# Performance work log

Hardware: AMD Instinct MI355X
Metric: run time of the kernel (lower is better)

## Reference

```python
import jax, jax.numpy as jnp
import numpy as np

B, LE, LS, DE, DS = 16, 1024, 1024, 1024, 1024


def setup_inputs() -> dict:
    key = jax.random.key(0)
    k1, k2, k3 = jax.random.split(key, 3)
    edit_encodings = jax.random.normal(k1, (B, LE, DE), dtype=jnp.float32)
    src_encodings = jax.random.normal(k2, (B, LS, DS), dtype=jnp.float32)
    # torch nn.Linear(DE, DS, bias=False) weight has shape (DS, DE)
    W = jax.random.normal(k3, (DS, DE), dtype=jnp.float32) * (1.0 / np.sqrt(DE))
    # padding masks: 1 for padding. Per-example valid lengths in [L/2, L].
    edit_lens = np.linspace(LE // 2, LE, B).astype(np.int32)
    src_lens = np.linspace(LS, LS // 2, B).astype(np.int32)
    edit_sent_masks = (np.arange(LE)[None, :] >= edit_lens[:, None]).astype(np.int32)
    src_sent_masks = (np.arange(LS)[None, :] >= src_lens[:, None]).astype(np.int32)
    return {
        "edit_encodings": edit_encodings,
        "src_encodings": src_encodings,
        "edit_sent_masks": jnp.asarray(edit_sent_masks),
        "src_sent_masks": jnp.asarray(src_sent_masks),
        "W": W,
    }


def reference(edit_encodings, src_encodings, edit_sent_masks, src_sent_masks, W):
    # sim: (B, LE, LS) = (edit @ W^T) @ src^T
    proj = jnp.einsum('bed,sd->bes', edit_encodings, W)          # (B, LE, DS)
    sim = jnp.einsum('bes,bls->bel', proj, src_encodings)        # (B, LE, LS)
    neg_inf = jnp.float32(-jnp.inf)
    edit_sim = jnp.where(src_sent_masks[:, None, :].astype(bool), neg_inf, sim)
    src_sim = jnp.where(edit_sent_masks[:, :, None].astype(bool), neg_inf, sim)
    edit_weights = jax.nn.softmax(edit_sim, axis=-1)             # over src positions
    src_weights = jax.nn.softmax(src_sim, axis=1)                # over edit positions
    edit_ctx = jnp.einsum('bel,bls->bes', edit_weights, src_encodings)  # (B, LE, DS)
    src_ctx = jnp.einsum('bel,bed->bld', src_weights, edit_encodings)   # (B, LS, DE)
    return (edit_ctx, src_ctx)
```

## Files before the change

### kernel.cpp

```cpp
#include <hip/hip_runtime.h>
#include <math.h>

#define BATCH 16

typedef __attribute__((ext_vector_type(8))) short s16x8;
typedef __attribute__((ext_vector_type(8))) unsigned short u16x8;
typedef __attribute__((ext_vector_type(4))) float f32x4;

__device__ inline unsigned short f2bf_rn(float f) {
  unsigned u = __float_as_uint(f);
  u += 0x7FFF + ((u >> 16) & 1);
  return (unsigned short)(u >> 16);
}
__device__ inline float bf2f(unsigned short h) {
  return __uint_as_float(((unsigned)h) << 16);
}

#define LDK 40

__global__ __launch_bounds__(256) void cvt_split(
    const float* __restrict__ X, unsigned short* __restrict__ H,
    unsigned short* __restrict__ L) {
  const size_t i = (((size_t)blockIdx.x << 8) + threadIdx.x) << 2;
  f32x4 v = *(const f32x4*)(X + i);
  ushort4 h, l;
  h.x = f2bf_rn(v[0]); l.x = f2bf_rn(v[0] - bf2f(h.x));
  h.y = f2bf_rn(v[1]); l.y = f2bf_rn(v[1] - bf2f(h.y));
  h.z = f2bf_rn(v[2]); l.z = f2bf_rn(v[2] - bf2f(h.z));
  h.w = f2bf_rn(v[3]); l.w = f2bf_rn(v[3] - bf2f(h.w));
  *(ushort4*)(H + i) = h;
  *(ushort4*)(L + i) = l;
}

template <int SPLIT_OUT>
__global__ __launch_bounds__(256) void gemm_split3b(
    const unsigned short* __restrict__ AH, const unsigned short* __restrict__ AL,
    const unsigned short* __restrict__ BH, const unsigned short* __restrict__ BL,
    void* __restrict__ Cout, void* __restrict__ CoutL,
    long long sA, long long sB, long long sC) {
  __shared__ unsigned short Ahs[128 * LDK], Als[128 * LDK];
  __shared__ unsigned short Bhs[128 * LDK], Bls[128 * LDK];
  const int z = blockIdx.z;
  const size_t oA = (size_t)z * sA, oB = (size_t)z * sB;
  const int tid = threadIdx.x;
  const int bm = blockIdx.x << 7, bn = blockIdx.y << 7;
  const int wave = tid >> 6, lane = tid & 63;
  const int wm = (wave & 1) << 6, wn = (wave >> 1) << 6;
  const int fr = lane & 15, fk = (lane >> 4) << 3;

  f32x4 acc[4][4];
#pragma unroll
  for (int i = 0; i < 4; i++)
#pragma unroll
    for (int j = 0; j < 4; j++) acc[i][j] = (f32x4)(0.f);

  const int sr = tid >> 1, sk = (tid & 1) << 4;
  const unsigned short* pAH = AH + oA + (size_t)(bm + sr) * 1024 + sk;
  const unsigned short* pAL = AL + oA + (size_t)(bm + sr) * 1024 + sk;
  const unsigned short* pBH = BH + oB + (size_t)(bn + sr) * 1024 + sk;
  const unsigned short* pBL = BL + oB + (size_t)(bn + sr) * 1024 + sk;
  unsigned short* wAh = &Ahs[sr * LDK + sk];
  unsigned short* wAl = &Als[sr * LDK + sk];
  unsigned short* wBh = &Bhs[sr * LDK + sk];
  unsigned short* wBl = &Bls[sr * LDK + sk];

#pragma unroll 1
  for (int k0 = 0; k0 < 1024; k0 += 32) {
    u16x8 ah0 = *(const u16x8*)(pAH + k0), ah1 = *(const u16x8*)(pAH + k0 + 8);
    u16x8 al0 = *(const u16x8*)(pAL + k0), al1 = *(const u16x8*)(pAL + k0 + 8);
    u16x8 bh0 = *(const u16x8*)(pBH + k0), bh1 = *(const u16x8*)(pBH + k0 + 8);
    u16x8 bl0 = *(const u16x8*)(pBL + k0), bl1 = *(const u16x8*)(pBL + k0 + 8);
    __syncthreads();
    *(u16x8*)(wAh) = ah0; *(u16x8*)(wAh + 8) = ah1;
    *(u16x8*)(wAl) = al0; *(u16x8*)(wAl + 8) = al1;
    *(u16x8*)(wBh) = bh0; *(u16x8*)(wBh + 8) = bh1;
    *(u16x8*)(wBl) = bl0; *(u16x8*)(wBl + 8) = bl1;
    __syncthreads();

    s16x8 ah[4], al[4];
#pragma unroll
    for (int i = 0; i < 4; i++) {
      const int ro = (wm + (i << 4) + fr) * LDK + fk;
      ah[i] = *(const s16x8*)&Ahs[ro];
      al[i] = *(const s16x8*)&Als[ro];
    }
#pragma unroll
    for (int j = 0; j < 4; j++) {
      const int ro = (wn + (j << 4) + fr) * LDK + fk;
      s16x8 bh = *(const s16x8*)&Bhs[ro];
      s16x8 bl = *(const s16x8*)&Bls[ro];
#pragma unroll
      for (int i = 0; i < 4; i++) {
        acc[i][j] = __builtin_amdgcn_mfma_f32_16x16x32_bf16(al[i], bh, acc[i][j], 0, 0, 0);
        acc[i][j] = __builtin_amdgcn_mfma_f32_16x16x32_bf16(ah[i], bl, acc[i][j], 0, 0, 0);
        acc[i][j] = __builtin_amdgcn_mfma_f32_16x16x32_bf16(ah[i], bh, acc[i][j], 0, 0, 0);
      }
    }
  }
  const int cr = (lane >> 4) << 2;
  if (SPLIT_OUT) {
    unsigned short* CH = (unsigned short*)Cout + (size_t)z * sC;
    unsigned short* CL = (unsigned short*)CoutL + (size_t)z * sC;
#pragma unroll
    for (int i = 0; i < 4; i++)
#pragma unroll
      for (int r = 0; r < 4; r++) {
        size_t base = (size_t)(bm + wm + (i << 4) + cr + r) * 1024 + bn + wn + fr;
#pragma unroll
        for (int j = 0; j < 4; j++) {
          float f = acc[i][j][r];
          unsigned short h = f2bf_rn(f);
          CH[base + (j << 4)] = h;
          CL[base + (j << 4)] = f2bf_rn(f - bf2f(h));
        }
      }
  } else {
    float* C = (float*)Cout + (size_t)z * sC;
#pragma unroll
    for (int i = 0; i < 4; i++)
#pragma unroll
      for (int r = 0; r < 4; r++) {
        float* cp = C + (size_t)(bm + wm + (i << 4) + cr + r) * 1024 + bn + wn + fr;
#pragma unroll
        for (int j = 0; j < 4; j++) cp[j << 4] = acc[i][j][r];
      }
  }
}

__global__ __launch_bounds__(256) void gemm_bf16(
    const unsigned short* __restrict__ A, const unsigned short* __restrict__ B,
    float* __restrict__ C, long long sA, long long sB, long long sC) {
  __shared__ unsigned short Ah[128 * LDK];
  __shared__ unsigned short Bh[128 * LDK];
  const int z = blockIdx.z;
  A += (size_t)z * sA; B += (size_t)z * sB; C += (size_t)z * sC;
  const int tid = threadIdx.x;
  const int bm = blockIdx.x << 7, bn = blockIdx.y << 7;
  const int wave = tid >> 6, lane = tid & 63;
  const int wm = (wave & 1) << 6, wn = (wave >> 1) << 6;
  const int fr = lane & 15, fk = (lane >> 4) << 3;

  f32x4 acc[4][4];
#pragma unroll
  for (int i = 0; i < 4; i++)
#pragma unroll
    for (int j = 0; j < 4; j++) acc[i][j] = (f32x4)(0.f);

  const int sr = tid >> 1, sk = (tid & 1) << 4;
  const unsigned short* pA = A + (size_t)(bm + sr) * 1024 + sk;
  const unsigned short* pB = B + (size_t)(bn + sr) * 1024 + sk;
  unsigned short* sAh = &Ah[sr * LDK + sk];
  unsigned short* sBh = &Bh[sr * LDK + sk];

#pragma unroll 1
  for (int k0 = 0; k0 < 1024; k0 += 32) {
    u16x8 a0 = *(const u16x8*)(pA + k0), a1 = *(const u16x8*)(pA + k0 + 8);
    u16x8 b0 = *(const u16x8*)(pB + k0), b1 = *(const u16x8*)(pB + k0 + 8);
    __syncthreads();
    *(u16x8*)(sAh) = a0; *(u16x8*)(sAh + 8) = a1;
    *(u16x8*)(sBh) = b0; *(u16x8*)(sBh + 8) = b1;
    __syncthreads();

    s16x8 ah[4];
#pragma unroll
    for (int i = 0; i < 4; i++)
      ah[i] = *(const s16x8*)&Ah[(wm + (i << 4) + fr) * LDK + fk];
#pragma unroll
    for (int j = 0; j < 4; j++) {
      s16x8 bh = *(const s16x8*)&Bh[(wn + (j << 4) + fr) * LDK + fk];
#pragma unroll
      for (int i = 0; i < 4; i++)
        acc[i][j] = __builtin_amdgcn_mfma_f32_16x16x32_bf16(ah[i], bh, acc[i][j], 0, 0, 0);
    }
  }
  const int cr = (lane >> 4) << 2;
#pragma unroll
  for (int i = 0; i < 4; i++)
#pragma unroll
    for (int r = 0; r < 4; r++) {
      float* cp = C + (size_t)(bm + wm + (i << 4) + cr + r) * 1024 + bn + wn + fr;
#pragma unroll
      for (int j = 0; j < 4; j++) cp[j << 4] = acc[i][j][r];
    }
}

__device__ inline float waveMax(float v) {
#pragma unroll
  for (int o = 32; o > 0; o >>= 1) v = fmaxf(v, __shfl_down(v, o, 64));
  return v;
}
__device__ inline float waveSum(float v) {
#pragma unroll
  for (int o = 32; o > 0; o >>= 1) v += __shfl_down(v, o, 64);
  return v;
}

__global__ __launch_bounds__(256) void row_softmax_kernel(
    const float* __restrict__ sim, const int* __restrict__ smask,
    unsigned short* __restrict__ out) {
  const int row = blockIdx.x;
  const int b = row >> 10;
  const float* x = sim + ((size_t)row << 10);
  const int* mk = smask + (b << 10);
  const int t = threadIdx.x;

  float4 v = ((const float4*)x)[t];
  int4 m = ((const int4*)mk)[t];
  float vv[4] = {v.x, v.y, v.z, v.w};
  const int mmv[4] = {m.x, m.y, m.z, m.w};

  float mx = -3.0e38f;
#pragma unroll
  for (int i = 0; i < 4; i++)
    if (!mmv[i]) mx = fmaxf(mx, vv[i]);

  __shared__ float red[4];
  float wmx = waveMax(mx);
  const int wave = t >> 6;
  if ((t & 63) == 0) red[wave] = wmx;
  __syncthreads();
  mx = fmaxf(fmaxf(red[0], red[1]), fmaxf(red[2], red[3]));
  __syncthreads();

  float s = 0.f;
#pragma unroll
  for (int i = 0; i < 4; i++) {
    float e = mmv[i] ? 0.f : __expf(vv[i] - mx);
    vv[i] = e;
    s += e;
  }
  float ws = waveSum(s);
  if ((t & 63) == 0) red[wave] = ws;
  __syncthreads();
  s = red[0] + red[1] + red[2] + red[3];
  float inv = 1.0f / s;

  ushort4 o;
  o.x = f2bf_rn(vv[0] * inv);
  o.y = f2bf_rn(vv[1] * inv);
  o.z = f2bf_rn(vv[2] * inv);
  o.w = f2bf_rn(vv[3] * inv);
  *(ushort4*)&out[((size_t)row << 10) + (t << 2)] = o;
}

__global__ __launch_bounds__(256) void col_partial(
    const float* __restrict__ sim, const int* __restrict__ emask,
    float* __restrict__ pmax, float* __restrict__ psum) {
  const int b = blockIdx.z;
  const int ec = blockIdx.y;
  const int l = (blockIdx.x << 8) + threadIdx.x;
  const float* p = sim + ((size_t)b << 20) + (((size_t)ec << 6) << 10) + l;
  const int* mk = emask + (b << 10) + (ec << 6);
  float mx0 = -1.0e30f, s0 = 0.f, mx1 = -1.0e30f, s1 = 0.f;
#pragma unroll 4
  for (int i = 0; i < 64; i += 2) {
    float v0 = mk[i] ? -3.0e38f : p[(size_t)i << 10];
    float v1 = mk[i + 1] ? -3.0e38f : p[(size_t)(i + 1) << 10];
    float n0 = fmaxf(mx0, v0);
    s0 = s0 * __expf(mx0 - n0) + __expf(v0 - n0);
    mx0 = n0;
    float n1 = fmaxf(mx1, v1);
    s1 = s1 * __expf(mx1 - n1) + __expf(v1 - n1);
    mx1 = n1;
  }
  float M = fmaxf(mx0, mx1);
  float S = s0 * __expf(mx0 - M) + s1 * __expf(mx1 - M);
  const int o = (((b << 4) + ec) << 10) + l;
  pmax[o] = M;
  psum[o] = S;
}

__global__ __launch_bounds__(256) void col_weights_T(
    const float* __restrict__ sim, const int* __restrict__ emask,
    const float* __restrict__ pmax, const float* __restrict__ psum,
    unsigned short* __restrict__ wT) {
  const int b = blockIdx.z;
  const int l0 = blockIdx.x << 6;
  const int e0 = blockIdx.y << 6;
  const int t = threadIdx.x;
  __shared__ float Ml[64], Il[64];
  __shared__ int msk[64];
  __shared__ float gm[4][64], gs[4][64];
  __shared__ unsigned short tile[64][72];

  {
    const int ll = t & 63, g = t >> 6;
    float m = -1.0e30f, s = 0.f;
#pragma unroll
    for (int q = 0; q < 4; q++) {
      int ec = g + (q << 2);
      const int o = (((b << 4) + ec) << 10) + l0 + ll;
      float pm = pmax[o], ps = psum[o];
      float nm = fmaxf(m, pm);
      s = s * __expf(m - nm) + ps * __expf(pm - nm);
      m = nm;
    }
    gm[g][ll] = m;
    gs[g][ll] = s;
    __syncthreads();
    if (t < 64) {
      float M = fmaxf(fmaxf(gm[0][t], gm[1][t]), fmaxf(gm[2][t], gm[3][t]));
      float S = 0.f;
#pragma unroll
      for (int q = 0; q < 4; q++) S += gs[q][t] * __expf(gm[q][t] - M);
      Ml[t] = M;
      Il[t] = 1.0f / S;
      msk[t] = emask[(b << 10) + e0 + t];
    }
    __syncthreads();
  }

  const int lane = t & 63, wv = t >> 6;
#pragma unroll
  for (int i = 0; i < 16; i++) {
    const int el = (wv << 4) + i;
    float v = sim[((size_t)b << 20) + ((size_t)(e0 + el) << 10) + l0 + lane];
    float w = msk[el] ? 0.f : __expf(v - Ml[lane]) * Il[lane];
    tile[lane][el] = f2bf_rn(w);
  }
  __syncthreads();
  const int r = t >> 2, seg = (t & 3) << 4;
  u16x8 v0 = *(const u16x8*)&tile[r][seg];
  u16x8 v1 = *(const u16x8*)&tile[r][seg + 8];
  size_t o = ((size_t)((b << 10) + l0 + r) << 10) + e0 + seg;
  *(u16x8*)&wT[o] = v0;
  *(u16x8*)&wT[o + 8] = v1;
}

__global__ __launch_bounds__(256) void transpose16(
    const unsigned short* __restrict__ X, unsigned short* __restrict__ XT) {
  __shared__ unsigned short ts[64][72];
  const int b = blockIdx.z;
  const int d0 = blockIdx.x << 6, l0 = blockIdx.y << 6;
  const int t = threadIdx.x;
  const unsigned short* Xb = X + ((size_t)b << 20);
  unsigned short* Tb = XT + ((size_t)b << 20);
  const int row = t >> 2, seg = (t & 3) << 4;
  u16x8 v0 = *(const u16x8*)&Xb[((size_t)(l0 + row) << 10) + d0 + seg];
  u16x8 v1 = *(const u16x8*)&Xb[((size_t)(l0 + row) << 10) + d0 + seg + 8];
#pragma unroll
  for (int i = 0; i < 8; i++) ts[seg + i][row] = v0[i];
#pragma unroll
  for (int i = 0; i < 8; i++) ts[seg + 8 + i][row] = v1[i];
  __syncthreads();
  u16x8 o0 = *(const u16x8*)&ts[row][seg];
  u16x8 o1 = *(const u16x8*)&ts[row][seg + 8];
  size_t o = ((size_t)(d0 + row) << 10) + l0 + seg;
  *(u16x8*)&Tb[o] = o0;
  *(u16x8*)&Tb[o + 8] = o1;
}

extern "C" void kernel_launch(void* const* d_in, const int* in_sizes, int n_in,
                              void* d_out, int out_size, void* d_ws,
                              size_t ws_size, hipStream_t stream) {
  const float* edit = (const float*)d_in[0];
  const float* src = (const float*)d_in[1];
  const int* emask = (const int*)d_in[2];
  const int* smask = (const int*)d_in[3];
  const float* W = (const float*)d_in[4];

  char* ws = (char*)d_ws;
  char* dob = (char*)d_out;

  unsigned short* eH = (unsigned short*)ws;
  unsigned short* sH = (unsigned short*)(ws + ((size_t)32 << 20));
  unsigned short* pH = (unsigned short*)(ws + ((size_t)64 << 20));
  unsigned short* pL = (unsigned short*)(ws + ((size_t)96 << 20));
  unsigned short* wE = pH;
  unsigned short* wST = pL;
  unsigned short* editT = sH;

  unsigned short* eL = (unsigned short*)dob;
  unsigned short* sL = (unsigned short*)(dob + ((size_t)64 << 20));
  unsigned short* WH = (unsigned short*)(dob + ((size_t)96 << 20));
  unsigned short* WL = (unsigned short*)(dob + ((size_t)98 << 20));
  float* sim = (float*)dob;
  float* pmax = (float*)(dob + ((size_t)64 << 20));
  float* psum = (float*)(dob + ((size_t)65 << 20));
  unsigned short* srcT = (unsigned short*)(dob + ((size_t)64 << 20));
  float* out_edit = (float*)dob;
  float* out_src = (float*)(dob + ((size_t)64 << 20));

  const long long S1 = 1LL << 20;
  dim3 blk(256);

  cvt_split<<<dim3(16384), blk, 0, stream>>>(edit, eH, eL);
  cvt_split<<<dim3(16384), blk, 0, stream>>>(src, sH, sL);
  cvt_split<<<dim3(1024), blk, 0, stream>>>(W, WH, WL);

  gemm_split3b<1><<<dim3(128, 8, 1), blk, 0, stream>>>(
      eH, eL, WH, WL, (void*)pH, (void*)pL, 0, 0, 0);

  gemm_split3b<0><<<dim3(8, 8, BATCH), blk, 0, stream>>>(
      pH, pL, sH, sL, (void*)sim, nullptr, S1, S1, S1);

  row_softmax_kernel<<<dim3(BATCH << 10), blk, 0, stream>>>(sim, smask, wE);
  col_partial<<<dim3(4, 16, BATCH), blk, 0, stream>>>(sim, emask, pmax, psum);
  col_weights_T<<<dim3(16, 16, BATCH), blk, 0, stream>>>(sim, emask, pmax, psum, wST);

  transpose16<<<dim3(16, 16, BATCH), blk, 0, stream>>>(sH, srcT);
  transpose16<<<dim3(16, 16, BATCH), blk, 0, stream>>>(eH, editT);

  gemm_bf16<<<dim3(8, 8, BATCH), blk, 0, stream>>>(wE, srcT, out_edit, S1, S1, S1);
  gemm_bf16<<<dim3(8, 8, BATCH), blk, 0, stream>>>(wST, editT, out_src, S1, S1, S1);
}
```

Measured before the change: 666.6 us.

## Use direct global-to-LDS loads with XOR swizzle and XCD-aware block remap in GEMMs

The GEMM kernels now stage tiles with global_load_lds (direct global-to-LDS DMA) instead of loading into registers and then writing to shared memory. The padded LDK=40 layout is replaced by an unpadded 32-wide layout with an XOR swizzle to avoid LDS bank conflicts. The grid is flattened to 1D and block indices are remapped so that consecutive tiles land on the same XCD, improving L2 reuse. The cost is a fixed swizzle mapping and a dependence on the global_load_lds builtin and its 16-byte width support.

```diff
diff --git a/kernel.cpp b/kernel.cpp
--- a/kernel.cpp
+++ b/kernel.cpp
@@ -16,7 +16,11 @@
   return __uint_as_float(((unsigned)h) << 16);
 }
 
-#define LDK 40
+__device__ __forceinline__ void gload16(const unsigned short* g, unsigned short* l) {
+  __builtin_amdgcn_global_load_lds(
+      (__attribute__((address_space(1))) void*)g,
+      (__attribute__((address_space(3))) void*)l, 16, 0, 0);
+}
 
 __global__ __launch_bounds__(256) void cvt_split(
     const float* __restrict__ X, unsigned short* __restrict__ H,
@@ -38,15 +42,20 @@
     const unsigned short* __restrict__ BH, const unsigned short* __restrict__ BL,
     void* __restrict__ Cout, void* __restrict__ CoutL,
     long long sA, long long sB, long long sC) {
-  __shared__ unsigned short Ahs[128 * LDK], Als[128 * LDK];
-  __shared__ unsigned short Bhs[128 * LDK], Bls[128 * LDK];
-  const int z = blockIdx.z;
+  __shared__ unsigned short Ahs[128 * 32], Als[128 * 32];
+  __shared__ unsigned short Bhs[128 * 32], Bls[128 * 32];
+  const int tid = threadIdx.x;
+  const int wg = ((blockIdx.x & 7) << 7) | (blockIdx.x >> 3);
+  int bm, bn, z;
+  if (SPLIT_OUT) {
+    z = 0; bm = (wg >> 3) << 7; bn = (wg & 7) << 7;
+  } else {
+    z = wg >> 6; bm = ((wg >> 3) & 7) << 7; bn = (wg & 7) << 7;
+  }
   const size_t oA = (size_t)z * sA, oB = (size_t)z * sB;
-  const int tid = threadIdx.x;
-  const int bm = blockIdx.x << 7, bn = blockIdx.y << 7;
   const int wave = tid >> 6, lane = tid & 63;
   const int wm = (wave & 1) << 6, wn = (wave >> 1) << 6;
-  const int fr = lane & 15, fk = (lane >> 4) << 3;
+  const int fr = lane & 15, fks = lane >> 4;
 
   f32x4 acc[4][4];
 #pragma unroll
@@ -54,41 +63,49 @@
 #pragma unroll
     for (int j = 0; j < 4; j++) acc[i][j] = (f32x4)(0.f);
 
-  const int sr = tid >> 1, sk = (tid & 1) << 4;
-  const unsigned short* pAH = AH + oA + (size_t)(bm + sr) * 1024 + sk;
-  const unsigned short* pAL = AL + oA + (size_t)(bm + sr) * 1024 + sk;
-  const unsigned short* pBH = BH + oB + (size_t)(bn + sr) * 1024 + sk;
-  const unsigned short* pBL = BL + oB + (size_t)(bn + sr) * 1024 + sk;
-  unsigned short* wAh = &Ahs[sr * LDK + sk];
-  unsigned short* wAl = &Als[sr * LDK + sk];
-  unsigned short* wBh = &Bhs[sr * LDK + sk];
-  unsigned short* wBl = &Bls[sr * LDK + sk];
+  const int srow = (wave << 5) + (lane >> 2);
+  const int gso = ((lane & 3) ^ ((srow >> 1) & 3)) << 3;
+  const unsigned short* gAH = AH + oA + (size_t)(bm + srow) * 1024 + gso;
+  const unsigned short* gAL = AL + oA + (size_t)(bm + srow) * 1024 + gso;
+  const unsigned short* gBH = BH + oB + (size_t)(bn + srow) * 1024 + gso;
+  const unsigned short* gBL = BL + oB + (size_t)(bn + srow) * 1024 + gso;
+  unsigned short* lAh = Ahs + (wave << 10);
+  unsigned short* lAl = Als + (wave << 10);
+  unsigned short* lBh = Bhs + (wave << 10);
+  unsigned short* lBl = Bls + (wave << 10);
+
+  int roA[4], roB[4];
+#pragma unroll
+  for (int i = 0; i < 4; i++) {
+    int rr = wm + (i << 4) + fr;
+    roA[i] = rr * 32 + ((fks ^ ((rr >> 1) & 3)) << 3);
+    rr = wn + (i << 4) + fr;
+    roB[i] = rr * 32 + ((fks ^ ((rr >> 1) & 3)) << 3);
+  }
 
 #pragma unroll 1
   for (int k0 = 0; k0 < 1024; k0 += 32) {
-    u16x8 ah0 = *(const u16x8*)(pAH + k0), ah1 = *(const u16x8*)(pAH + k0 + 8);
-    u16x8 al0 = *(const u16x8*)(pAL + k0), al1 = *(const u16x8*)(pAL + k0 + 8);
-    u16x8 bh0 = *(const u16x8*)(pBH + k0), bh1 = *(const u16x8*)(pBH + k0 + 8);
-    u16x8 bl0 = *(const u16x8*)(pBL + k0), bl1 = *(const u16x8*)(pBL + k0 + 8);
-    __syncthreads();
-    *(u16x8*)(wAh) = ah0; *(u16x8*)(wAh + 8) = ah1;
-    *(u16x8*)(wAl) = al0; *(u16x8*)(wAl + 8) = al1;
-    *(u16x8*)(wBh) = bh0; *(u16x8*)(wBh + 8) = bh1;
-    *(u16x8*)(wBl) = bl0; *(u16x8*)(wBl + 8) = bl1;
+    __syncthreads();
+    gload16(gAH + k0, lAh);
+    gload16(gAH + k0 + 16384, lAh + 512);
+    gload16(gAL + k0, lAl);
+    gload16(gAL + k0 + 16384, lAl + 512);
+    gload16(gBH + k0, lBh);
+    gload16(gBH + k0 + 16384, lBh + 512);
+    gload16(gBL + k0, lBl);
+    gload16(gBL + k0 + 16384, lBl + 512);
     __syncthreads();
 
     s16x8 ah[4], al[4];
 #pragma unroll
     for (int i = 0; i < 4; i++) {
-      const int ro = (wm + (i << 4) + fr) * LDK + fk;
-      ah[i] = *(const s16x8*)&Ahs[ro];
-      al[i] = *(const s16x8*)&Als[ro];
+      ah[i] = *(const s16x8*)&Ahs[roA[i]];
+      al[i] = *(const s16x8*)&Als[roA[i]];
     }
 #pragma unroll
     for (int j = 0; j < 4; j++) {
-      const int ro = (wn + (j << 4) + fr) * LDK + fk;
-      s16x8 bh = *(const s16x8*)&Bhs[ro];
-      s16x8 bl = *(const s16x8*)&Bls[ro];
+      s16x8 bh = *(const s16x8*)&Bhs[roB[j]];
+      s16x8 bl = *(const s16x8*)&Bls[roB[j]];
 #pragma unroll
       for (int i = 0; i < 4; i++) {
         acc[i][j] = __builtin_amdgcn_mfma_f32_16x16x32_bf16(al[i], bh, acc[i][j], 0, 0, 0);
@@ -130,15 +147,16 @@
 __global__ __launch_bounds__(256) void gemm_bf16(
     const unsigned short* __restrict__ A, const unsigned short* __restrict__ B,
     float* __restrict__ C, long long sA, long long sB, long long sC) {
-  __shared__ unsigned short Ah[128 * LDK];
-  __shared__ unsigned short Bh[128 * LDK];
-  const int z = blockIdx.z;
+  __shared__ unsigned short Ahs[128 * 32];
+  __shared__ unsigned short Bhs[128 * 32];
+  const int tid = threadIdx.x;
+  const int wg = ((blockIdx.x & 7) << 7) | (blockIdx.x >> 3);
+  const int z = wg >> 6;
+  const int bm = ((wg >> 3) & 7) << 7, bn = (wg & 7) << 7;
   A += (size_t)z * sA; B += (size_t)z * sB; C += (size_t)z * sC;
-  const int tid = threadIdx.x;
-  const int bm = blockIdx.x << 7, bn = blockIdx.y << 7;
   const int wave = tid >> 6, lane = tid & 63;
   const int wm = (wave & 1) << 6, wn = (wave >> 1) << 6;
-  const int fr = lane & 15, fk = (lane >> 4) << 3;
+  const int fr = lane & 15, fks = lane >> 4;
 
   f32x4 acc[4][4];
 #pragma unroll
@@ -146,28 +164,37 @@
 #pragma unroll
     for (int j = 0; j < 4; j++) acc[i][j] = (f32x4)(0.f);
 
-  const int sr = tid >> 1, sk = (tid & 1) << 4;
-  const unsigned short* pA = A + (size_t)(bm + sr) * 1024 + sk;
-  const unsigned short* pB = B + (size_t)(bn + sr) * 1024 + sk;
-  unsigned short* sAh = &Ah[sr * LDK + sk];
-  unsigned short* sBh = &Bh[sr * LDK + sk];
+  const int srow = (wave << 5) + (lane >> 2);
+  const int gso = ((lane & 3) ^ ((srow >> 1) & 3)) << 3;
+  const unsigned short* gA = A + (size_t)(bm + srow) * 1024 + gso;
+  const unsigned short* gB = B + (size_t)(bn + srow) * 1024 + gso;
+  unsigned short* lA = Ahs + (wave << 10);
+  unsigned short* lB = Bhs + (wave << 10);
+
+  int roA[4], roB[4];
+#pragma unroll
+  for (int i = 0; i < 4; i++) {
+    int rr = wm + (i << 4) + fr;
+    roA[i] = rr * 32 + ((fks ^ ((rr >> 1) & 3)) << 3);
+    rr = wn + (i << 4) + fr;
+    roB[i] = rr * 32 + ((fks ^ ((rr >> 1) & 3)) << 3);
+  }
 
 #pragma unroll 1
   for (int k0 = 0; k0 < 1024; k0 += 32) {
-    u16x8 a0 = *(const u16x8*)(pA + k0), a1 = *(const u16x8*)(pA + k0 + 8);
-    u16x8 b0 = *(const u16x8*)(pB + k0), b1 = *(const u16x8*)(pB + k0 + 8);
-    __syncthreads();
-    *(u16x8*)(sAh) = a0; *(u16x8*)(sAh + 8) = a1;
-    *(u16x8*)(sBh) = b0; *(u16x8*)(sBh + 8) = b1;
+    __syncthreads();
+    gload16(gA + k0, lA);
+    gload16(gA + k0 + 16384, lA + 512);
+    gload16(gB + k0, lB);
+    gload16(gB + k0 + 16384, lB + 512);
     __syncthreads();
 
     s16x8 ah[4];
 #pragma unroll
-    for (int i = 0; i < 4; i++)
-      ah[i] = *(const s16x8*)&Ah[(wm + (i << 4) + fr) * LDK + fk];
+    for (int i = 0; i < 4; i++) ah[i] = *(const s16x8*)&Ahs[roA[i]];
 #pragma unroll
     for (int j = 0; j < 4; j++) {
-      s16x8 bh = *(const s16x8*)&Bh[(wn + (j << 4) + fr) * LDK + fk];
+      s16x8 bh = *(const s16x8*)&Bhs[roB[j]];
 #pragma unroll
       for (int i = 0; i < 4; i++)
         acc[i][j] = __builtin_amdgcn_mfma_f32_16x16x32_bf16(ah[i], bh, acc[i][j], 0, 0, 0);
@@ -388,10 +415,10 @@
   cvt_split<<<dim3(16384), blk, 0, stream>>>(src, sH, sL);
   cvt_split<<<dim3(1024), blk, 0, stream>>>(W, WH, WL);
 
-  gemm_split3b<1><<<dim3(128, 8, 1), blk, 0, stream>>>(
+  gemm_split3b<1><<<dim3(1024), blk, 0, stream>>>(
       eH, eL, WH, WL, (void*)pH, (void*)pL, 0, 0, 0);
 
-  gemm_split3b<0><<<dim3(8, 8, BATCH), blk, 0, stream>>>(
+  gemm_split3b<0><<<dim3(1024), blk, 0, stream>>>(
       pH, pL, sH, sL, (void*)sim, nullptr, S1, S1, S1);
 
   row_softmax_kernel<<<dim3(BATCH << 10), blk, 0, stream>>>(sim, smask, wE);
@@ -401,6 +428,6 @@
   transpose16<<<dim3(16, 16, BATCH), blk, 0, stream>>>(sH, srcT);
   transpose16<<<dim3(16, 16, BATCH), blk, 0, stream>>>(eH, editT);
 
-  gemm_bf16<<<dim3(8, 8, BATCH), blk, 0, stream>>>(wE, srcT, out_edit, S1, S1, S1);
-  gemm_bf16<<<dim3(8, 8, BATCH), blk, 0, stream>>>(wST, editT, out_src, S1, S1, S1);
-}
+  gemm_bf16<<<dim3(1024), blk, 0, stream>>>(wE, srcT, out_edit, S1, S1, S1);
+  gemm_bf16<<<dim3(1024), blk, 0, stream>>>(wST, editT, out_src, S1, S1, S1);
+}
```

After: 621.9 us. 6.7% less time.

## Replace GEMMs with 256x256 double-buffered direct-to-LDS MFMA kernel and merge launches

Applied to the files above, without the earlier changes.

Replaces both GEMM kernels with one templated 512-thread kernel that computes 256x256 tiles. It double-buffers LDS through global_load_lds, uses an XOR-swizzled LDS layout, interleaves prefetch with MFMA phases using s_barrier and setprio, and remaps block indices for locality. It also merges the two conversion launches and the two transpose launches into single kernels. The aim is more data reuse per tile, hiding global load latency and cutting launch overhead. The cost is higher register and LDS use, and only 256 workgroups per GEMM, which may leave some CUs underused.

```diff
diff --git a/kernel.cpp b/kernel.cpp
--- a/kernel.cpp
+++ b/kernel.cpp
@@ -16,7 +16,11 @@
   return __uint_as_float(((unsigned)h) << 16);
 }
 
-#define LDK 40
+__device__ __forceinline__ void gload16(const unsigned short* g, unsigned short* l) {
+  __builtin_amdgcn_global_load_lds(
+      (__attribute__((address_space(1))) void*)g,
+      (__attribute__((address_space(3))) void*)l, 16, 0, 0);
+}
 
 __global__ __launch_bounds__(256) void cvt_split(
     const float* __restrict__ X, unsigned short* __restrict__ H,
@@ -32,156 +36,190 @@
   *(ushort4*)(L + i) = l;
 }
 
-template <int SPLIT_OUT>
-__global__ __launch_bounds__(256) void gemm_split3b(
+__global__ __launch_bounds__(256) void cvt_split2(
+    const float* __restrict__ X0, unsigned short* __restrict__ H0,
+    unsigned short* __restrict__ L0, const float* __restrict__ X1,
+    unsigned short* __restrict__ H1, unsigned short* __restrict__ L1) {
+  const int bid = blockIdx.x;
+  const float* X;
+  unsigned short *H, *L;
+  size_t base;
+  if (bid < 16384) { X = X0; H = H0; L = L0; base = (size_t)bid << 8; }
+  else { X = X1; H = H1; L = L1; base = (size_t)(bid - 16384) << 8; }
+  const size_t i = (base + threadIdx.x) << 2;
+  f32x4 v = *(const f32x4*)(X + i);
+  ushort4 h, l;
+  h.x = f2bf_rn(v[0]); l.x = f2bf_rn(v[0] - bf2f(h.x));
+  h.y = f2bf_rn(v[1]); l.y = f2bf_rn(v[1] - bf2f(h.y));
+  h.z = f2bf_rn(v[2]); l.z = f2bf_rn(v[2] - bf2f(h.z));
+  h.w = f2bf_rn(v[3]); l.w = f2bf_rn(v[3] - bf2f(h.w));
+  *(ushort4*)(H + i) = h;
+  *(ushort4*)(L + i) = l;
+}
+
+template <int HILO, int SPLIT_OUT>
+__global__ __launch_bounds__(512, 2) void gemm8p(
     const unsigned short* __restrict__ AH, const unsigned short* __restrict__ AL,
     const unsigned short* __restrict__ BH, const unsigned short* __restrict__ BL,
     void* __restrict__ Cout, void* __restrict__ CoutL,
-    long long sA, long long sB, long long sC) {
-  __shared__ unsigned short Ahs[128 * LDK], Als[128 * LDK];
-  __shared__ unsigned short Bhs[128 * LDK], Bls[128 * LDK];
-  const int z = blockIdx.z;
-  const size_t oA = (size_t)z * sA, oB = (size_t)z * sB;
+    long long sA, long long sB, long long sC, int batched) {
+  constexpr int NARR = HILO ? 4 : 2;
+  __shared__ __align__(16) unsigned short lds[2][NARR][8192];
   const int tid = threadIdx.x;
-  const int bm = blockIdx.x << 7, bn = blockIdx.y << 7;
+  const int wg = ((blockIdx.x & 7) << 5) | (blockIdx.x >> 3);
+  int z, bm, bn;
+  if (batched) {
+    z = wg >> 4; bm = ((wg >> 2) & 3) << 8; bn = (wg & 3) << 8;
+  } else {
+    z = 0; bm = (wg >> 2) << 8; bn = (wg & 3) << 8;
+  }
   const int wave = tid >> 6, lane = tid & 63;
-  const int wm = (wave & 1) << 6, wn = (wave >> 1) << 6;
-  const int fr = lane & 15, fk = (lane >> 4) << 3;
-
-  f32x4 acc[4][4];
-#pragma unroll
-  for (int i = 0; i < 4; i++)
-#pragma unroll
-    for (int j = 0; j < 4; j++) acc[i][j] = (f32x4)(0.f);
-
-  const int sr = tid >> 1, sk = (tid & 1) << 4;
-  const unsigned short* pAH = AH + oA + (size_t)(bm + sr) * 1024 + sk;
-  const unsigned short* pAL = AL + oA + (size_t)(bm + sr) * 1024 + sk;
-  const unsigned short* pBH = BH + oB + (size_t)(bn + sr) * 1024 + sk;
-  const unsigned short* pBL = BL + oB + (size_t)(bn + sr) * 1024 + sk;
-  unsigned short* wAh = &Ahs[sr * LDK + sk];
-  unsigned short* wAl = &Als[sr * LDK + sk];
-  unsigned short* wBh = &Bhs[sr * LDK + sk];
-  unsigned short* wBl = &Bls[sr * LDK + sk];
+  const int wm = wave >> 2, wn = wave & 3;
+  const int fr = lane & 15, fks = lane >> 4;
+
+  const int svrow = tid >> 2;
+  const int scol = ((tid & 3) ^ ((tid >> 3) & 3)) << 3;
+  const unsigned short* gA0 = AH + (size_t)z * sA + (size_t)(bm + svrow) * 1024 + scol;
+  const unsigned short* gB0 = BH + (size_t)z * sB + (size_t)(bn + svrow) * 1024 + scol;
+  const unsigned short* gA1 = HILO ? (AL + (size_t)z * sA + (size_t)(bm + svrow) * 1024 + scol) : gA0;
+  const unsigned short* gB1 = HILO ? (BL + (size_t)z * sB + (size_t)(bn + svrow) * 1024 + scol) : gB0;
+  const int lwb = wave << 9;
+
+  int aoff[8], boff[4];
+#pragma unroll
+  for (int m = 0; m < 8; m++) {
+    const int r = (wm << 7) + (m << 4) + fr;
+    aoff[m] = (r << 5) + ((fks ^ ((r >> 1) & 3)) << 3);
+  }
+#pragma unroll
+  for (int n = 0; n < 4; n++) {
+    const int r = (wn << 6) + (n << 4) + fr;
+    boff[n] = (r << 5) + ((fks ^ ((r >> 1) & 3)) << 3);
+  }
+
+  f32x4 acc[8][4];
+#pragma unroll
+  for (int m = 0; m < 8; m++)
+#pragma unroll
+    for (int n = 0; n < 4; n++) acc[m][n] = (f32x4)(0.f);
+
+#define ISS(NXT, ARR, G, Q, KO) \
+  gload16((G) + ((size_t)(Q) << 17) + (KO), &lds[NXT][ARR][((Q) << 12) + lwb])
+
+  ISS(0, 0, gA0, 0, 0); ISS(0, 0, gA0, 1, 0);
+  ISS(0, 1, gB0, 0, 0); ISS(0, 1, gB0, 1, 0);
+  if (HILO) {
+    ISS(0, 2, gA1, 0, 0); ISS(0, 2, gA1, 1, 0);
+    ISS(0, 3, gB1, 0, 0); ISS(0, 3, gB1, 1, 0);
+  }
+  __syncthreads();
 
 #pragma unroll 1
-  for (int k0 = 0; k0 < 1024; k0 += 32) {
-    u16x8 ah0 = *(const u16x8*)(pAH + k0), ah1 = *(const u16x8*)(pAH + k0 + 8);
-    u16x8 al0 = *(const u16x8*)(pAL + k0), al1 = *(const u16x8*)(pAL + k0 + 8);
-    u16x8 bh0 = *(const u16x8*)(pBH + k0), bh1 = *(const u16x8*)(pBH + k0 + 8);
-    u16x8 bl0 = *(const u16x8*)(pBL + k0), bl1 = *(const u16x8*)(pBL + k0 + 8);
+  for (int kt = 0; kt < 32; ++kt) {
+    const int cur = kt & 1, nxt = cur ^ 1;
+    const int kn = (kt + 1) << 5;
+    const bool pf = kt < 31;
+    const unsigned short* LAH = lds[cur][0];
+    const unsigned short* LBH = lds[cur][1];
+    const unsigned short* LAL = lds[cur][HILO ? 2 : 0];
+    const unsigned short* LBL = lds[cur][HILO ? 3 : 1];
+    s16x8 ah[4], al[4], bh[2], bl[2];
+
+#define LDA8(QM)                                                         \
+  do {                                                                   \
+    _Pragma("unroll") for (int m_ = 0; m_ < 4; m_++) {                   \
+      const int o_ = aoff[((QM) << 2) + m_];                             \
+      ah[m_] = *(const s16x8*)&LAH[o_];                                  \
+      if (HILO) al[m_] = *(const s16x8*)&LAL[o_];                        \
+    }                                                                    \
+  } while (0)
+#define LDB4(QN)                                                         \
+  do {                                                                   \
+    _Pragma("unroll") for (int n_ = 0; n_ < 2; n_++) {                   \
+      const int o_ = boff[((QN) << 1) + n_];                             \
+      bh[n_] = *(const s16x8*)&LBH[o_];                                  \
+      if (HILO) bl[n_] = *(const s16x8*)&LBL[o_];                        \
+    }                                                                    \
+  } while (0)
+#define MM8(QM, QN)                                                              \
+  do {                                                                           \
+    _Pragma("unroll") for (int m_ = 0; m_ < 4; m_++)                             \
+        _Pragma("unroll") for (int n_ = 0; n_ < 2; n_++) {                       \
+      const int M_ = ((QM) << 2) + m_, N_ = ((QN) << 1) + n_;                    \
+      if (HILO) {                                                                \
+        acc[M_][N_] = __builtin_amdgcn_mfma_f32_16x16x32_bf16(al[m_], bh[n_],    \
+                                                              acc[M_][N_], 0, 0, 0); \
+        acc[M_][N_] = __builtin_amdgcn_mfma_f32_16x16x32_bf16(ah[m_], bl[n_],    \
+                                                              acc[M_][N_], 0, 0, 0); \
+      }                                                                          \
+      acc[M_][N_] = __builtin_amdgcn_mfma_f32_16x16x32_bf16(ah[m_], bh[n_],      \
+                                                            acc[M_][N_], 0, 0, 0);   \
+    }                                                                            \
+  } while (0)
+
+    LDA8(0); LDB4(0);
+    if (pf) {
+      ISS(nxt, 0, gA0, 0, kn); ISS(nxt, 0, gA0, 1, kn);
+      if (HILO) { ISS(nxt, 2, gA1, 0, kn); ISS(nxt, 2, gA1, 1, kn); }
+    }
+    __builtin_amdgcn_s_barrier();
+    __builtin_amdgcn_s_setprio(1); MM8(0, 0); __builtin_amdgcn_s_setprio(0);
+    __builtin_amdgcn_s_barrier();
+
+    LDB4(1);
+    if (pf) {
+      ISS(nxt, 1, gB0, 0, kn); ISS(nxt, 1, gB0, 1, kn);
+      if (HILO) { ISS(nxt, 3, gB1, 0, kn); ISS(nxt, 3, gB1, 1, kn); }
+    }
+    __builtin_amdgcn_s_barrier();
+    __builtin_amdgcn_s_setprio(1); MM8(0, 1); __builtin_amdgcn_s_setprio(0);
+    __builtin_amdgcn_s_barrier();
+
+    LDA8(1); LDB4(0);
+    __builtin_amdgcn_s_barrier();
+    __builtin_amdgcn_s_setprio(1); MM8(1, 0); __builtin_amdgcn_s_setprio(0);
+    __builtin_amdgcn_s_barrier();
+
+    LDB4(1);
+    __builtin_amdgcn_s_barrier();
+    __builtin_amdgcn_s_setprio(1); MM8(1, 1); __builtin_amdgcn_s_setprio(0);
     __syncthreads();
-    *(u16x8*)(wAh) = ah0; *(u16x8*)(wAh + 8) = ah1;
-    *(u16x8*)(wAl) = al0; *(u16x8*)(wAl + 8) = al1;
-    *(u16x8*)(wBh) = bh0; *(u16x8*)(wBh + 8) = bh1;
-    *(u16x8*)(wBl) = bl0; *(u16x8*)(wBl + 8) = bl1;
-    __syncthreads();
-
-    s16x8 ah[4], al[4];
-#pragma unroll
-    for (int i = 0; i < 4; i++) {
-      const int ro = (wm + (i << 4) + fr) * LDK + fk;
-      ah[i] = *(const s16x8*)&Ahs[ro];
-      al[i] = *(const s16x8*)&Als[ro];
-    }
-#pragma unroll
-    for (int j = 0; j < 4; j++) {
-      const int ro = (wn + (j << 4) + fr) * LDK + fk;
-      s16x8 bh = *(const s16x8*)&Bhs[ro];
-      s16x8 bl = *(const s16x8*)&Bls[ro];
-#pragma unroll
-      for (int i = 0; i < 4; i++) {
-        acc[i][j] = __builtin_amdgcn_mfma_f32_16x16x32_bf16(al[i], bh, acc[i][j], 0, 0, 0);
-        acc[i][j] = __builtin_amdgcn_mfma_f32_16x16x32_bf16(ah[i], bl, acc[i][j], 0, 0, 0);
-        acc[i][j] = __builtin_amdgcn_mfma_f32_16x16x32_bf16(ah[i], bh, acc[i][j], 0, 0, 0);
-      }
-    }
-  }
+#undef LDA8
+#undef LDB4
+#undef MM8
+  }
+#undef ISS
+
   const int cr = (lane >> 4) << 2;
+  const int crow0 = bm + (wm << 7);
+  const int ccol0 = bn + (wn << 6);
   if (SPLIT_OUT) {
     unsigned short* CH = (unsigned short*)Cout + (size_t)z * sC;
     unsigned short* CL = (unsigned short*)CoutL + (size_t)z * sC;
 #pragma unroll
-    for (int i = 0; i < 4; i++)
+    for (int m = 0; m < 8; m++)
 #pragma unroll
       for (int r = 0; r < 4; r++) {
-        size_t base = (size_t)(bm + wm + (i << 4) + cr + r) * 1024 + bn + wn + fr;
-#pragma unroll
-        for (int j = 0; j < 4; j++) {
-          float f = acc[i][j][r];
+        const size_t base = (size_t)(crow0 + (m << 4) + cr + r) * 1024 + ccol0 + fr;
+#pragma unroll
+        for (int n = 0; n < 4; n++) {
+          float f = acc[m][n][r];
           unsigned short h = f2bf_rn(f);
-          CH[base + (j << 4)] = h;
-          CL[base + (j << 4)] = f2bf_rn(f - bf2f(h));
+          CH[base + (n << 4)] = h;
+          CL[base + (n << 4)] = f2bf_rn(f - bf2f(h));
         }
       }
   } else {
     float* C = (float*)Cout + (size_t)z * sC;
 #pragma unroll
-    for (int i = 0; i < 4; i++)
+    for (int m = 0; m < 8; m++)
 #pragma unroll
       for (int r = 0; r < 4; r++) {
-        float* cp = C + (size_t)(bm + wm + (i << 4) + cr + r) * 1024 + bn + wn + fr;
-#pragma unroll
-        for (int j = 0; j < 4; j++) cp[j << 4] = acc[i][j][r];
+        float* cp = C + (size_t)(crow0 + (m << 4) + cr + r) * 1024 + ccol0 + fr;
+#pragma unroll
+        for (int n = 0; n < 4; n++) cp[n << 4] = acc[m][n][r];
       }
   }
-}
-
-__global__ __launch_bounds__(256) void gemm_bf16(
-    const unsigned short* __restrict__ A, const unsigned short* __restrict__ B,
-    float* __restrict__ C, long long sA, long long sB, long long sC) {
-  __shared__ unsigned short Ah[128 * LDK];
-  __shared__ unsigned short Bh[128 * LDK];
-  const int z = blockIdx.z;
-  A += (size_t)z * sA; B += (size_t)z * sB; C += (size_t)z * sC;
-  const int tid = threadIdx.x;
-  const int bm = blockIdx.x << 7, bn = blockIdx.y << 7;
-  const int wave = tid >> 6, lane = tid & 63;
-  const int wm = (wave & 1) << 6, wn = (wave >> 1) << 6;
-  const int fr = lane & 15, fk = (lane >> 4) << 3;
-
-  f32x4 acc[4][4];
-#pragma unroll
-  for (int i = 0; i < 4; i++)
-#pragma unroll
-    for (int j = 0; j < 4; j++) acc[i][j] = (f32x4)(0.f);
-
-  const int sr = tid >> 1, sk = (tid & 1) << 4;
-  const unsigned short* pA = A + (size_t)(bm + sr) * 1024 + sk;
-  const unsigned short* pB = B + (size_t)(bn + sr) * 1024 + sk;
-  unsigned short* sAh = &Ah[sr * LDK + sk];
-  unsigned short* sBh = &Bh[sr * LDK + sk];
-
-#pragma unroll 1
-  for (int k0 = 0; k0 < 1024; k0 += 32) {
-    u16x8 a0 = *(const u16x8*)(pA + k0), a1 = *(const u16x8*)(pA + k0 + 8);
-    u16x8 b0 = *(const u16x8*)(pB + k0), b1 = *(const u16x8*)(pB + k0 + 8);
-    __syncthreads();
-    *(u16x8*)(sAh) = a0; *(u16x8*)(sAh + 8) = a1;
-    *(u16x8*)(sBh) = b0; *(u16x8*)(sBh + 8) = b1;
-    __syncthreads();
-
-    s16x8 ah[4];
-#pragma unroll
-    for (int i = 0; i < 4; i++)
-      ah[i] = *(const s16x8*)&Ah[(wm + (i << 4) + fr) * LDK + fk];
-#pragma unroll
-    for (int j = 0; j < 4; j++) {
-      s16x8 bh = *(const s16x8*)&Bh[(wn + (j << 4) + fr) * LDK + fk];
-#pragma unroll
-      for (int i = 0; i < 4; i++)
-        acc[i][j] = __builtin_amdgcn_mfma_f32_16x16x32_bf16(ah[i], bh, acc[i][j], 0, 0, 0);
-    }
-  }
-  const int cr = (lane >> 4) << 2;
-#pragma unroll
-  for (int i = 0; i < 4; i++)
-#pragma unroll
-    for (int r = 0; r < 4; r++) {
-      float* cp = C + (size_t)(bm + wm + (i << 4) + cr + r) * 1024 + bn + wn + fr;
-#pragma unroll
-      for (int j = 0; j < 4; j++) cp[j << 4] = acc[i][j][r];
-    }
 }
 
 __device__ inline float waveMax(float v) {
@@ -327,14 +365,16 @@
   *(u16x8*)&wT[o + 8] = v1;
 }
 
-__global__ __launch_bounds__(256) void transpose16(
-    const unsigned short* __restrict__ X, unsigned short* __restrict__ XT) {
+__global__ __launch_bounds__(256) void transpose16d(
+    const unsigned short* __restrict__ X0, unsigned short* __restrict__ T0,
+    const unsigned short* __restrict__ X1, unsigned short* __restrict__ T1) {
   __shared__ unsigned short ts[64][72];
-  const int b = blockIdx.z;
+  const int zz = blockIdx.z;
+  const int b = zz & 15;
+  const unsigned short* Xb = (zz < 16 ? X0 : X1) + ((size_t)b << 20);
+  unsigned short* Tb = (zz < 16 ? T0 : T1) + ((size_t)b << 20);
   const int d0 = blockIdx.x << 6, l0 = blockIdx.y << 6;
   const int t = threadIdx.x;
-  const unsigned short* Xb = X + ((size_t)b << 20);
-  unsigned short* Tb = XT + ((size_t)b << 20);
   const int row = t >> 2, seg = (t & 3) << 4;
   u16x8 v0 = *(const u16x8*)&Xb[((size_t)(l0 + row) << 10) + d0 + seg];
   u16x8 v1 = *(const u16x8*)&Xb[((size_t)(l0 + row) << 10) + d0 + seg + 8];
@@ -382,25 +422,25 @@
   float* out_src = (float*)(dob + ((size_t)64 << 20));
 
   const long long S1 = 1LL << 20;
-  dim3 blk(256);
-
-  cvt_split<<<dim3(16384), blk, 0, stream>>>(edit, eH, eL);
-  cvt_split<<<dim3(16384), blk, 0, stream>>>(src, sH, sL);
+  dim3 blk(256), blk512(512);
+
+  cvt_split2<<<dim3(32768), blk, 0, stream>>>(edit, eH, eL, src, sH, sL);
   cvt_split<<<dim3(1024), blk, 0, stream>>>(W, WH, WL);
 
-  gemm_split3b<1><<<dim3(128, 8, 1), blk, 0, stream>>>(
-      eH, eL, WH, WL, (void*)pH, (void*)pL, 0, 0, 0);
-
-  gemm_split3b<0><<<dim3(8, 8, BATCH), blk, 0, stream>>>(
-      pH, pL, sH, sL, (void*)sim, nullptr, S1, S1, S1);
+  gemm8p<1, 1><<<dim3(256), blk512, 0, stream>>>(
+      eH, eL, WH, WL, (void*)pH, (void*)pL, 0, 0, 0, 0);
+
+  gemm8p<1, 0><<<dim3(256), blk512, 0, stream>>>(
+      pH, pL, sH, sL, (void*)sim, nullptr, S1, S1, S1, 1);
 
   row_softmax_kernel<<<dim3(BATCH << 10), blk, 0, stream>>>(sim, smask, wE);
   col_partial<<<dim3(4, 16, BATCH), blk, 0, stream>>>(sim, emask, pmax, psum);
   col_weights_T<<<dim3(16, 16, BATCH), blk, 0, stream>>>(sim, emask, pmax, psum, wST);
 
-  transpose16<<<dim3(16, 16, BATCH), blk, 0, stream>>>(sH, srcT);
-  transpose16<<<dim3(16, 16, BATCH), blk, 0, stream>>>(eH, editT);
-
-  gemm_bf16<<<dim3(8, 8, BATCH), blk, 0, stream>>>(wE, srcT, out_edit, S1, S1, S1);
-  gemm_bf16<<<dim3(8, 8, BATCH), blk, 0, stream>>>(wST, editT, out_src, S1, S1, S1);
-}
+  transpose16d<<<dim3(16, 16, 32), blk, 0, stream>>>(sH, srcT, eH, editT);
+
+  gemm8p<0, 0><<<dim3(256), blk512, 0, stream>>>(
+      wE, nullptr, srcT, nullptr, (void*)out_edit, nullptr, S1, S1, S1, 1);
+  gemm8p<0, 0><<<dim3(256), blk512, 0, stream>>>(
+      wST, nullptr, editT, nullptr, (void*)out_src, nullptr, S1, S1, S1, 1);
+}
```

New measurement: 549.7 us. 17.5% less time.
